# Performance work log

Measured on AMD Instinct MI355X. Metric: run time of the kernel, lower is better.

The kernel has to match this reference:

```python
import jax, jax.numpy as jnp
import numpy as np

DIM = 1024
HEADS = 16
EPS = 1e-05
B, T, C, H, W = 2, 16, DIM, 32, 32


def setup_inputs() -> dict:
    key = jax.random.key(0)
    ks = jax.random.split(key, 4)
    s = 1.0 / np.sqrt(DIM)
    return {
        "x": jax.random.normal(ks[0], (B, T, C, H, W), dtype=jnp.float32),
        "ln_w": jnp.ones((C,), dtype=jnp.float32),
        "ln_b": jnp.zeros((C,), dtype=jnp.float32),
        "Wq": jax.random.normal(ks[1], (C, C), dtype=jnp.float32) * s,
        "Wk": jax.random.normal(ks[2], (C, C), dtype=jnp.float32) * s,
        "Wv": jax.random.normal(ks[3], (C, C), dtype=jnp.float32) * s,
    }


def reference(x, ln_w, ln_b, Wq, Wk, Wv):
    b, t, c, h, w = x.shape
    heads = HEADS
    dh = c // heads
    scale = dh ** (-0.5)

    # Channel LayerNorm: normalize over C per (b,t,h,w)
    xc = jnp.transpose(x, (0, 1, 3, 4, 2))  # [B,T,H,W,C]
    mu = jnp.mean(xc, axis=-1, keepdims=True)
    var = jnp.mean(jnp.square(xc - mu), axis=-1, keepdims=True)
    xn = (xc - mu) * jax.lax.rsqrt(var + EPS) * ln_w + ln_b  # [B,T,H,W,C]

    # Q/K from spatial mean-pool
    pooled = jnp.mean(xn, axis=(2, 3))  # [B,T,C]
    q = pooled @ Wq.T  # [B,T,C]
    k = pooled @ Wk.T  # [B,T,C]

    # V per pixel; torch permutes to [B,W,H,T,C] then flattens W-major
    v = jnp.transpose(xn, (0, 3, 2, 1, 4)).reshape(b, h * w, t, c)  # [B,HW(w-major),T,C]
    v = v @ Wv.T

    q = q.reshape(b, t, heads, dh).transpose(0, 2, 1, 3) * scale  # [B,h,T,dh]
    k = k.reshape(b, t, heads, dh).transpose(0, 2, 3, 1)          # [B,h,dh,T]
    v = v.reshape(b, h * w, t, heads, dh).transpose(0, 1, 3, 2, 4)  # [B,HW,h,T,dh]

    attn = jax.nn.softmax(jnp.matmul(q, k), axis=-1)  # [B,h,T,T]
    out = jnp.einsum('bhst,bnhtd->bnhsd', attn, v)    # [B,HW,h,T,dh]
    # permute(0,3,2,4,1) -> [B,T,h,dh,HW], then view as (H,W)
    out = out.transpose(0, 3, 2, 4, 1).reshape(b, t, c, h, w)
    return out
```

## Files before the change

kernel.cpp:

```cpp
#include <hip/hip_runtime.h>
#include <stdint.h>
#include <stddef.h>

#define CDIM 1024
#define HWD  1024
#define TD   16
#define BD   2
#define NH   16
#define DHD  64

typedef __attribute__((ext_vector_type(8))) short bf16x8;
typedef __attribute__((ext_vector_type(4))) short bf16x4;
typedef __attribute__((ext_vector_type(4))) float f32x4;

static __device__ __forceinline__ short f2bf(float f) {
  uint32_t u = __builtin_bit_cast(uint32_t, f);
  uint32_t r = (u + 0x7FFFu + ((u >> 16) & 1u)) >> 16;
  return (short)(uint16_t)r;
}
static __device__ __forceinline__ float bf2f(short s) {
  return __builtin_bit_cast(float, (uint32_t)((uint16_t)s) << 16);
}

static __device__ __forceinline__ void gl_lds16(const short* g, short* l) {
  __builtin_amdgcn_global_load_lds((const __attribute__((address_space(1))) unsigned int*)g,
                                   (__attribute__((address_space(3))) unsigned int*)l,
                                   16, 0, 0);
}

__global__ void k_cast3(const float* __restrict__ Wq, const float* __restrict__ Wk,
                        const float* __restrict__ Wv, short* __restrict__ Wqkb,
                        short* __restrict__ Wb) {
  int bid = blockIdx.x;
  int mat = bid >> 10;
  const float* src = mat == 0 ? Wq : (mat == 1 ? Wk : Wv);
  short* dst = mat == 0 ? Wqkb : (mat == 1 ? Wqkb + 1048576 : Wb);
  int i = ((bid & 1023) * 256 + threadIdx.x) * 4;
  f32x4 v = *(const f32x4*)&src[i];
  dst[i + 0] = f2bf(v[0]);
  dst[i + 1] = f2bf(v[1]);
  dst[i + 2] = f2bf(v[2]);
  dst[i + 3] = f2bf(v[3]);
}

__global__ __launch_bounds__(256) void k_ln(const float* __restrict__ x,
                                            const float* __restrict__ lnw,
                                            const float* __restrict__ lnb,
                                            short* __restrict__ xnT,
                                            float* __restrict__ part) {
  int bt = blockIdx.y;
  int pg = blockIdx.x;
  int P0 = pg * 32;
  int tid = threadIdx.x;
  int pq = tid & 7, cr = tid >> 3;
  const float* xs = x + (size_t)bt * CDIM * HWD;
  short* outB = xnT + (size_t)bt * CDIM * HWD;

  f32x4 v[32];
  float s[4] = {}, s2[4] = {};
  #pragma unroll
  for (int j = 0; j < 32; ++j) {
    int c = cr + 32 * j;
    v[j] = *(const f32x4*)&xs[(size_t)c * HWD + P0 + pq * 4];
    #pragma unroll
    for (int i = 0; i < 4; ++i) { s[i] += v[j][i]; s2[i] += v[j][i] * v[j][i]; }
  }
  __shared__ float redA[32][33], redB[32][33];
  #pragma unroll
  for (int i = 0; i < 4; ++i) {
    redA[cr][pq * 4 + i] = s[i];
    redB[cr][pq * 4 + i] = s2[i];
  }
  __syncthreads();
  __shared__ float muS[32], rsS[32];
  if (tid < 32) {
    float a = 0.f, b2 = 0.f;
    #pragma unroll
    for (int k = 0; k < 32; ++k) { a += redA[k][tid]; b2 += redB[k][tid]; }
    float mu = a * (1.0f / CDIM);
    float var = b2 * (1.0f / CDIM) - mu * mu;
    muS[tid] = mu;
    rsS[tid] = rsqrtf(var + 1e-5f);
  }
  __syncthreads();
  float mu_[4], rs_[4];
  #pragma unroll
  for (int i = 0; i < 4; ++i) { mu_[i] = muS[pq * 4 + i]; rs_[i] = rsS[pq * 4 + i]; }

  __shared__ short tile[32 * 514];
  __shared__ float prA[512][8];

  #pragma unroll
  for (int ch = 0; ch < 2; ++ch) {
    #pragma unroll
    for (int jj = 0; jj < 16; ++jj) {
      int j = ch * 16 + jj;
      int cl = cr + 32 * jj;
      int c = ch * 512 + cl;
      float w = lnw[c], bb = lnb[c];
      int cc = cl >> 3, c7 = cl & 7;
      float psum = 0.f;
      #pragma unroll
      for (int i = 0; i < 4; ++i) {
        int px = pq * 4 + i;
        float xn = (v[j][i] - mu_[i]) * rs_[i] * w + bb;
        psum += xn;
        tile[px * 514 + ((cc ^ (px & 7)) << 3) + c7] = f2bf(xn);
      }
      prA[cl][pq] = psum;
    }
    __syncthreads();
    {
      int qr = tid & 31, seg = tid >> 5;
      int q = qr * 32 + pg;
      short* dst = outB + (size_t)q * CDIM + ch * 512 + seg * 64;
      #pragma unroll
      for (int mm = 0; mm < 8; ++mm) {
        int cc = seg * 8 + mm;
        bf16x8 vv = *(const bf16x8*)&tile[qr * 514 + ((cc ^ (qr & 7)) << 3)];
        *(bf16x8*)&dst[mm * 8] = vv;
      }
    }
    #pragma unroll
    for (int rep = 0; rep < 2; ++rep) {
      int cl = rep * 256 + tid;
      float a = 0.f;
      #pragma unroll
      for (int k = 0; k < 8; ++k) a += prA[cl][k];
      part[((size_t)(bt * 32 + pg)) * CDIM + ch * 512 + cl] = a;
    }
    __syncthreads();
  }
}

__global__ void k_pool_red(const float* __restrict__ part, short* __restrict__ pooledb) {
  int bt = blockIdx.y;
  int c = blockIdx.x * 256 + threadIdx.x;
  float s = 0.f;
  #pragma unroll
  for (int pc = 0; pc < 32; ++pc) s += part[((size_t)(bt * 32 + pc)) * CDIM + c];
  pooledb[bt * CDIM + c] = f2bf(s * (1.0f / HWD));
}

__global__ __launch_bounds__(256) void k_qk_mfma(const short* __restrict__ Wqkb,
                                                 const short* __restrict__ pooledb,
                                                 float* __restrict__ qm,
                                                 float* __restrict__ km) {
  int n0 = blockIdx.x * 128;
  __shared__ __align__(16) short lA[32 * 32];
  __shared__ __align__(16) short lB[128 * 32];
  int tid = threadIdx.x, lane = tid & 63, wid = tid >> 6;
  int s0 = wid * 128 + lane, s1 = s0 + 64;
  int fr = lane & 15, fk = (lane >> 4) * 8;
  f32x4 acc[2][2] = {};

  for (int kt = 0; kt < CDIM / 32; ++kt) {
    int k0 = kt * 32;
    __syncthreads();
    gl_lds16(&Wqkb[(size_t)(n0 + (s0 >> 2)) * CDIM + k0 + (s0 & 3) * 8], &lB[s0 * 8]);
    gl_lds16(&Wqkb[(size_t)(n0 + (s1 >> 2)) * CDIM + k0 + (s1 & 3) * 8], &lB[s1 * 8]);
    if (wid < 2) {
      gl_lds16(&pooledb[(size_t)(tid >> 2) * CDIM + k0 + (tid & 3) * 8], &lA[tid * 8]);
    }
    __syncthreads();
    bf16x8 af[2], bfr[2];
    #pragma unroll
    for (int mi = 0; mi < 2; ++mi)
      af[mi] = *(const bf16x8*)&lA[(mi * 16 + fr) * 32 + fk];
    #pragma unroll
    for (int ni = 0; ni < 2; ++ni)
      bfr[ni] = *(const bf16x8*)&lB[(wid * 32 + ni * 16 + fr) * 32 + fk];
    #pragma unroll
    for (int mi = 0; mi < 2; ++mi)
      #pragma unroll
      for (int ni = 0; ni < 2; ++ni)
        acc[mi][ni] = __builtin_amdgcn_mfma_f32_16x16x32_bf16(af[mi], bfr[ni], acc[mi][ni], 0, 0, 0);
  }

  int cr = lane >> 4;
  #pragma unroll
  for (int mi = 0; mi < 2; ++mi)
    #pragma unroll
    for (int ni = 0; ni < 2; ++ni)
      #pragma unroll
      for (int rr = 0; rr < 4; ++rr) {
        int row = mi * 16 + cr * 4 + rr;
        int col = n0 + wid * 32 + ni * 16 + fr;
        float v = acc[mi][ni][rr];
        if (col < 1024) qm[(size_t)row * CDIM + col] = v;
        else            km[(size_t)row * CDIM + col - 1024] = v;
      }
}

__global__ void k_attn(const float* __restrict__ qm, const float* __restrict__ km,
                       float* __restrict__ attn) {
  int bg = blockIdx.x;
  int b = bg >> 4, g = bg & 15;
  int s = threadIdx.x >> 4, t = threadIdx.x & 15;
  const float* qr = qm + (size_t)(b * TD + s) * CDIM + g * DHD;
  const float* kr = km + (size_t)(b * TD + t) * CDIM + g * DHD;
  float d = 0.f;
  #pragma unroll
  for (int i = 0; i < DHD; ++i) d += qr[i] * kr[i];
  d *= 0.125f;
  float m = d;
  #pragma unroll
  for (int off = 8; off; off >>= 1) m = fmaxf(m, __shfl_xor(m, off, 16));
  float e = __expf(d - m);
  float sum = e;
  #pragma unroll
  for (int off = 8; off; off >>= 1) sum += __shfl_xor(sum, off, 16);
  attn[(size_t)bg * 256 + s * 16 + t] = e / sum;
}

__global__ __launch_bounds__(512, 2) void k_vgemm(const short* __restrict__ Wb,
                                                  const short* __restrict__ xnT,
                                                  short* __restrict__ vp) {
  int bid = blockIdx.x;
  int swz = (bid & 7) * 64 + (bid >> 3);
  int bt = swz >> 4;
  int m0 = ((swz >> 2) & 3) * 256;
  int n0 = (swz & 3) * 256;
  const short* Bm = xnT + (size_t)bt * CDIM * HWD;

  __shared__ __align__(16) short lA[2][256 * 64];
  __shared__ __align__(16) short lB[2][256 * 64];

  int tid = threadIdx.x, lane = tid & 63, wid = tid >> 6;
  int wm = wid >> 2, wn = wid & 3;

  int srow = wid * 8 + (lane >> 3);
  int schunk = (lane & 7) ^ (lane >> 3);
  const short* gA = Wb + (size_t)(m0 + srow) * CDIM + schunk * 8;
  const short* gB = Bm + (size_t)(n0 + srow) * CDIM + schunk * 8;
  int doff = wid * 512 + lane * 8;

  int fr = lane & 15, klane = lane >> 4;
  int c0 = ((klane ^ (fr & 7)) * 8);
  int rA = (wm * 128 + fr) * 64;
  int rB = (wn * 64 + fr) * 64;

  f32x4 acc[8][4] = {};
  bf16x8 bq[4], af[4];

#define ISSUE(p, kt1, nb)                                                      \
  do {                                                                         \
    gl_lds16(gA + (size_t)(p) * 64 * CDIM + (kt1) * 64, &lA[nb][(p) * 4096 + doff]); \
    gl_lds16(gB + (size_t)(p) * 64 * CDIM + (kt1) * 64, &lB[nb][(p) * 4096 + doff]); \
  } while (0)
#define RDA(mi, ks, b) (*(const bf16x8*)&lA[b][rA + (mi) * 1024 + (c0 ^ ((ks) * 32))])
#define RDB(ni, ks, b) (*(const bf16x8*)&lB[b][rB + (ni) * 1024 + (c0 ^ ((ks) * 32))])

  ISSUE(0, 0, 0); ISSUE(1, 0, 0); ISSUE(2, 0, 0); ISSUE(3, 0, 0);

  for (int kt = 0; kt < 16; ++kt) {
    int cur = kt & 1, nxt = cur ^ 1;
    bool st = (kt + 1 < 16);
    if (st) {
      ISSUE(0, kt + 1, nxt);
      asm volatile("s_waitcnt vmcnt(2)" ::: "memory");
    } else {
      asm volatile("s_waitcnt vmcnt(0)" ::: "memory");
    }
    __builtin_amdgcn_s_barrier();
    #pragma unroll
    for (int ni = 0; ni < 4; ++ni) bq[ni] = RDB(ni, 0, cur);
    #pragma unroll
    for (int mi = 0; mi < 4; ++mi) af[mi] = RDA(mi, 0, cur);
    __builtin_amdgcn_s_setprio(1);
    #pragma unroll
    for (int mi = 0; mi < 4; ++mi)
      #pragma unroll
      for (int ni = 0; ni < 4; ++ni)
        acc[mi][ni] = __builtin_amdgcn_mfma_f32_16x16x32_bf16(af[mi], bq[ni], acc[mi][ni], 0, 0, 0);
    __builtin_amdgcn_s_setprio(0);
    __builtin_amdgcn_s_barrier();
    #pragma unroll
    for (int mi = 0; mi < 4; ++mi) af[mi] = RDA(4 + mi, 0, cur);
    if (st) ISSUE(1, kt + 1, nxt);
    __builtin_amdgcn_s_barrier();
    __builtin_amdgcn_s_setprio(1);
    #pragma unroll
    for (int mi = 0; mi < 4; ++mi)
      #pragma unroll
      for (int ni = 0; ni < 4; ++ni)
        acc[4 + mi][ni] = __builtin_amdgcn_mfma_f32_16x16x32_bf16(af[mi], bq[ni], acc[4 + mi][ni], 0, 0, 0);
    __builtin_amdgcn_s_setprio(0);
    __builtin_amdgcn_s_barrier();
    #pragma unroll
    for (int ni = 0; ni < 4; ++ni) bq[ni] = RDB(ni, 1, cur);
    #pragma unroll
    for (int mi = 0; mi < 4; ++mi) af[mi] = RDA(mi, 1, cur);
    if (st) ISSUE(2, kt + 1, nxt);
    __builtin_amdgcn_s_barrier();
    __builtin_amdgcn_s_setprio(1);
    #pragma unroll
    for (int mi = 0; mi < 4; ++mi)
      #pragma unroll
      for (int ni = 0; ni < 4; ++ni)
        acc[mi][ni] = __builtin_amdgcn_mfma_f32_16x16x32_bf16(af[mi], bq[ni], acc[mi][ni], 0, 0, 0);
    __builtin_amdgcn_s_setprio(0);
    __builtin_amdgcn_s_barrier();
    #pragma unroll
    for (int mi = 0; mi < 4; ++mi) af[mi] = RDA(4 + mi, 1, cur);
    if (st) ISSUE(3, kt + 1, nxt);
    __builtin_amdgcn_s_barrier();
    __builtin_amdgcn_s_setprio(1);
    #pragma unroll
    for (int mi = 0; mi < 4; ++mi)
      #pragma unroll
      for (int ni = 0; ni < 4; ++ni)
        acc[4 + mi][ni] = __builtin_amdgcn_mfma_f32_16x16x32_bf16(af[mi], bq[ni], acc[4 + mi][ni], 0, 0, 0);
    __builtin_amdgcn_s_setprio(0);
    __builtin_amdgcn_s_barrier();
  }
#undef ISSUE
#undef RDA
#undef RDB

  short* outB = vp + (size_t)bt * CDIM * HWD;
  int cr = lane >> 4;
  #pragma unroll
  for (int mi = 0; mi < 8; ++mi)
    #pragma unroll
    for (int ni = 0; ni < 4; ++ni)
      #pragma unroll
      for (int r = 0; r < 4; ++r) {
        int row = m0 + wm * 128 + mi * 16 + cr * 4 + r;
        int col = n0 + wn * 64 + ni * 16 + fr;
        outB[(size_t)row * HWD + col] = f2bf(acc[mi][ni][r]);
      }
}

__global__ __launch_bounds__(256) void k_mix(const short* __restrict__ vp,
                                             const float* __restrict__ attn,
                                             float* __restrict__ out) {
  int c = blockIdx.x;
  int b = blockIdx.y;
  int g = c >> 6;
  __shared__ __align__(16) short vpl[TD * HWD];
  __shared__ float at[256];
  int tid = threadIdx.x;
  at[tid] = attn[(size_t)(b * NH + g) * 256 + tid];
  #pragma unroll
  for (int j = 0; j < 8; ++j) {
    int chunk = j * 256 + tid;
    int t = chunk >> 7, qc = chunk & 127;
    bf16x8 v = *(const bf16x8*)&vp[((size_t)(b * TD + t) * CDIM + c) * HWD + qc * 8];
    *(bf16x8*)&vpl[t * HWD + qc * 8] = v;
  }
  __syncthreads();
  int p = tid * 4;
  #pragma unroll
  for (int sh = 0; sh < 2; ++sh) {
    f32x4 acc[8] = {};
    #pragma unroll
    for (int t = 0; t < TD; ++t) {
      bf16x4 v4 = *(const bf16x4*)&vpl[t * HWD + p];
      f32x4 vf = {bf2f(v4[0]), bf2f(v4[1]), bf2f(v4[2]), bf2f(v4[3])};
      #pragma unroll
      for (int s8 = 0; s8 < 8; ++s8) {
        float a = at[(sh * 8 + s8) * 16 + t];
        acc[s8] += a * vf;
      }
    }
    #pragma unroll
    for (int s8 = 0; s8 < 8; ++s8) {
      int s = sh * 8 + s8;
      *(f32x4*)&out[((size_t)(b * TD + s) * CDIM + c) * HWD + p] = acc[s8];
    }
  }
}

extern "C" void kernel_launch(void* const* d_in, const int* in_sizes, int n_in,
                              void* d_out, int out_size, void* d_ws, size_t ws_size,
                              hipStream_t stream) {
  const float* x   = (const float*)d_in[0];
  const float* lnw = (const float*)d_in[1];
  const float* lnb = (const float*)d_in[2];
  const float* Wq  = (const float*)d_in[3];
  const float* Wk  = (const float*)d_in[4];
  const float* Wv  = (const float*)d_in[5];
  float* out = (float*)d_out;

  char* ws = (char*)d_ws;
  const size_t XNT_OFF   = 0;
  const size_t VP_OFF    = XNT_OFF + 67108864;
  const size_t WB_OFF    = VP_OFF + 67108864;
  const size_t WQKB_OFF  = WB_OFF + 2097152;
  const size_t POOLB_OFF = WQKB_OFF + 4194304;
  const size_t QM_OFF    = POOLB_OFF + 65536;
  const size_t KM_OFF    = QM_OFF + 131072;
  const size_t ATTN_OFF  = KM_OFF + 131072;

  short* xnT    = (short*)(ws + XNT_OFF);
  short* vp     = (short*)(ws + VP_OFF);
  float* part   = (float*)(ws + VP_OFF);
  short* Wb     = (short*)(ws + WB_OFF);
  short* Wqkb   = (short*)(ws + WQKB_OFF);
  short* poolb  = (short*)(ws + POOLB_OFF);
  float* qm     = (float*)(ws + QM_OFF);
  float* km     = (float*)(ws + KM_OFF);
  float* attn   = (float*)(ws + ATTN_OFF);

  k_cast3<<<dim3(3072), 256, 0, stream>>>(Wq, Wk, Wv, Wqkb, Wb);
  k_ln<<<dim3(32, 32), 256, 0, stream>>>(x, lnw, lnb, xnT, part);
  k_pool_red<<<dim3(4, 32), 256, 0, stream>>>(part, poolb);
  k_qk_mfma<<<dim3(16), 256, 0, stream>>>(Wqkb, poolb, qm, km);
  k_attn<<<dim3(32), 256, 0, stream>>>(qm, km, attn);
  k_vgemm<<<dim3(512), 512, 0, stream>>>(Wb, xnT, vp);
  k_mix<<<dim3(1024, 2), 256, 0, stream>>>(vp, attn, out);
}
```

Before: 195.4 us.

## Rework LayerNorm kernel to re-read x instead of holding it in registers

The LayerNorm kernel no longer keeps all 32 f32x4 values per thread in registers between the statistics pass and the normalize pass. It re-reads x from global memory in 128-channel chunks, and it now uses 512-thread blocks covering 64 pixels with a smaller aliased LDS buffer. The pooled partial sums now come from wavefront shuffles instead of an LDS reduction array, which halves the number of partial slices that the pool reduction reads. The aim is to cut register and LDS pressure so more waves fit per CU. The cost is reading x twice (an extra 128 MB of traffic, possibly served from cache) and four times as many transpose/store phases and barriers.

```diff
diff --git a/kernel.cpp b/kernel.cpp
--- a/kernel.cpp
+++ b/kernel.cpp
@@ -43,40 +43,44 @@
   dst[i + 3] = f2bf(v[3]);
 }
 
-__global__ __launch_bounds__(256) void k_ln(const float* __restrict__ x,
+__global__ __launch_bounds__(512) void k_ln(const float* __restrict__ x,
                                             const float* __restrict__ lnw,
                                             const float* __restrict__ lnb,
                                             short* __restrict__ xnT,
                                             float* __restrict__ part) {
   int bt = blockIdx.y;
   int pg = blockIdx.x;
-  int P0 = pg * 32;
+  int P0 = pg * 64;
   int tid = threadIdx.x;
-  int pq = tid & 7, cr = tid >> 3;
+  int pq = tid & 15, cr = tid >> 4;
+  int pbase = P0 + pq * 4;
   const float* xs = x + (size_t)bt * CDIM * HWD;
   short* outB = xnT + (size_t)bt * CDIM * HWD;
 
-  f32x4 v[32];
+  __shared__ __align__(16) char lbuf[2 * 32 * 65 * 4];
+  float* redA = (float*)lbuf;
+  float* redB = redA + 32 * 65;
+  short* tile = (short*)lbuf;
+  __shared__ float muS[64], rsS[64];
+
   float s[4] = {}, s2[4] = {};
   #pragma unroll
   for (int j = 0; j < 32; ++j) {
     int c = cr + 32 * j;
-    v[j] = *(const f32x4*)&xs[(size_t)c * HWD + P0 + pq * 4];
-    #pragma unroll
-    for (int i = 0; i < 4; ++i) { s[i] += v[j][i]; s2[i] += v[j][i] * v[j][i]; }
-  }
-  __shared__ float redA[32][33], redB[32][33];
+    f32x4 v = *(const f32x4*)&xs[(size_t)c * HWD + pbase];
+    #pragma unroll
+    for (int i = 0; i < 4; ++i) { s[i] += v[i]; s2[i] += v[i] * v[i]; }
+  }
   #pragma unroll
   for (int i = 0; i < 4; ++i) {
-    redA[cr][pq * 4 + i] = s[i];
-    redB[cr][pq * 4 + i] = s2[i];
+    redA[cr * 65 + pq * 4 + i] = s[i];
+    redB[cr * 65 + pq * 4 + i] = s2[i];
   }
   __syncthreads();
-  __shared__ float muS[32], rsS[32];
-  if (tid < 32) {
+  if (tid < 64) {
     float a = 0.f, b2 = 0.f;
     #pragma unroll
-    for (int k = 0; k < 32; ++k) { a += redA[k][tid]; b2 += redB[k][tid]; }
+    for (int k = 0; k < 32; ++k) { a += redA[k * 65 + tid]; b2 += redB[k * 65 + tid]; }
     float mu = a * (1.0f / CDIM);
     float var = b2 * (1.0f / CDIM) - mu * mu;
     muS[tid] = mu;
@@ -87,47 +91,40 @@
   #pragma unroll
   for (int i = 0; i < 4; ++i) { mu_[i] = muS[pq * 4 + i]; rs_[i] = rsS[pq * 4 + i]; }
 
-  __shared__ short tile[32 * 514];
-  __shared__ float prA[512][8];
-
-  #pragma unroll
-  for (int ch = 0; ch < 2; ++ch) {
-    #pragma unroll
-    for (int jj = 0; jj < 16; ++jj) {
-      int j = ch * 16 + jj;
+  for (int h = 0; h < 8; ++h) {
+    #pragma unroll
+    for (int jj = 0; jj < 4; ++jj) {
       int cl = cr + 32 * jj;
-      int c = ch * 512 + cl;
+      int c = h * 128 + cl;
+      f32x4 v = *(const f32x4*)&xs[(size_t)c * HWD + pbase];
       float w = lnw[c], bb = lnb[c];
       int cc = cl >> 3, c7 = cl & 7;
       float psum = 0.f;
       #pragma unroll
       for (int i = 0; i < 4; ++i) {
         int px = pq * 4 + i;
-        float xn = (v[j][i] - mu_[i]) * rs_[i] * w + bb;
+        float xn = (v[i] - mu_[i]) * rs_[i] * w + bb;
         psum += xn;
-        tile[px * 514 + ((cc ^ (px & 7)) << 3) + c7] = f2bf(xn);
+        tile[px * 130 + ((cc ^ (px & 7)) << 3) + c7] = f2bf(xn);
       }
-      prA[cl][pq] = psum;
+      psum += __shfl_xor(psum, 1, 64);
+      psum += __shfl_xor(psum, 2, 64);
+      psum += __shfl_xor(psum, 4, 64);
+      psum += __shfl_xor(psum, 8, 64);
+      if (pq == 0)
+        part[((size_t)(bt * 16 + pg)) * CDIM + c] = psum;
     }
     __syncthreads();
     {
-      int qr = tid & 31, seg = tid >> 5;
-      int q = qr * 32 + pg;
-      short* dst = outB + (size_t)q * CDIM + ch * 512 + seg * 64;
-      #pragma unroll
-      for (int mm = 0; mm < 8; ++mm) {
-        int cc = seg * 8 + mm;
-        bf16x8 vv = *(const bf16x8*)&tile[qr * 514 + ((cc ^ (qr & 7)) << 3)];
+      int qr = tid & 63, sg = tid >> 6;
+      int q = (qr & 31) * 32 + pg * 2 + (qr >> 5);
+      short* dst = outB + (size_t)q * CDIM + h * 128 + sg * 16;
+      #pragma unroll
+      for (int mm = 0; mm < 2; ++mm) {
+        int cc = sg * 2 + mm;
+        bf16x8 vv = *(const bf16x8*)&tile[qr * 130 + ((cc ^ (qr & 7)) << 3)];
         *(bf16x8*)&dst[mm * 8] = vv;
       }
-    }
-    #pragma unroll
-    for (int rep = 0; rep < 2; ++rep) {
-      int cl = rep * 256 + tid;
-      float a = 0.f;
-      #pragma unroll
-      for (int k = 0; k < 8; ++k) a += prA[cl][k];
-      part[((size_t)(bt * 32 + pg)) * CDIM + ch * 512 + cl] = a;
     }
     __syncthreads();
   }
@@ -138,7 +135,7 @@
   int c = blockIdx.x * 256 + threadIdx.x;
   float s = 0.f;
   #pragma unroll
-  for (int pc = 0; pc < 32; ++pc) s += part[((size_t)(bt * 32 + pc)) * CDIM + c];
+  for (int pc = 0; pc < 16; ++pc) s += part[((size_t)(bt * 16 + pc)) * CDIM + c];
   pooledb[bt * CDIM + c] = f2bf(s * (1.0f / HWD));
 }
 
@@ -404,7 +401,7 @@
   float* attn   = (float*)(ws + ATTN_OFF);
 
   k_cast3<<<dim3(3072), 256, 0, stream>>>(Wq, Wk, Wv, Wqkb, Wb);
-  k_ln<<<dim3(32, 32), 256, 0, stream>>>(x, lnw, lnb, xnT, part);
+  k_ln<<<dim3(16, 32), 512, 0, stream>>>(x, lnw, lnb, xnT, part);
   k_pool_red<<<dim3(4, 32), 256, 0, stream>>>(part, poolb);
   k_qk_mfma<<<dim3(16), 256, 0, stream>>>(Wqkb, poolb, qm, km);
   k_attn<<<dim3(32), 256, 0, stream>>>(qm, km, attn);
```

Result: slower. 222.2 us (+13.7%).
